# Optimization experiments

Measured on AMD Instinct MI355X. Metric: run time of the kernel, lower is better.

Reference implementation:

```python
import jax, jax.numpy as jnp
import numpy as np

# Izhikevich constants (module defaults)
A, B_P, C_P, D_P = 0.02, 0.2, -65.0, 8.0
V_TH, DT, T_STEPS = 30.0, 0.5, 8
LN_EPS = 1e-5

IN_F, OUT_F, BATCH = 4096, 4096, 256


def setup_inputs() -> dict:
    key = jax.random.key(0)
    k_x, k_w, k_n = jax.random.split(key, 3)
    x = jax.random.normal(k_x, (BATCH, IN_F), dtype=jnp.float32)
    # kaiming_normal_ fan_in / relu: std = sqrt(2 / fan_in)
    W = jax.random.normal(k_w, (OUT_F, IN_F), dtype=jnp.float32) * np.sqrt(2.0 / IN_F)
    b = jnp.zeros((OUT_F,), dtype=jnp.float32)
    ln_gamma = jnp.ones((OUT_F,), dtype=jnp.float32)
    ln_beta = jnp.zeros((OUT_F,), dtype=jnp.float32)
    current_mag = jnp.asarray(12.0, dtype=jnp.float32)
    # per-step injected noise, precomputed for determinism: (T, B, N)
    noise = jax.random.normal(k_n, (T_STEPS, BATCH, OUT_F), dtype=jnp.float32)
    return {"x": x, "W": W, "b": b, "ln_gamma": ln_gamma, "ln_beta": ln_beta,
            "current_mag": current_mag, "noise": noise}


@jax.custom_vjp
def superspike(v):
    return (v >= V_TH).astype(v.dtype)

def _ss_fwd(v):
    return superspike(v), v

def _ss_bwd(v, g):
    return (g / (1.0 + jnp.abs(v - V_TH)) ** 2,)

superspike.defvjp(_ss_fwd, _ss_bwd)


def reference(x, W, b, ln_gamma, ln_beta, current_mag, noise):
    # 1. Linear projection: (B, in) @ (in, out)
    raw = x @ W.T + b
    # 2. LayerNorm -> tanh -> scale to pA range
    mu = jnp.mean(raw, axis=-1, keepdims=True)
    var = jnp.mean(jnp.square(raw - mu), axis=-1, keepdims=True)
    ln = (raw - mu) * jax.lax.rsqrt(var + LN_EPS) * ln_gamma + ln_beta
    I_inj = jnp.tanh(ln) * jnp.abs(current_mag)  # (B, N)

    B = x.shape[0]
    v0 = jnp.full((B, OUT_F), -65.0, dtype=x.dtype)
    u0 = jnp.full((B, OUT_F), B_P * -65.0, dtype=x.dtype)

    def step(carry, noise_t):
        v, u = carry
        I_t = I_inj + 0.3 * noise_t
        dv = (0.04 * v * v + 5.0 * v + 140.0 - u + I_t) * DT
        du = A * (B_P * v - u) * DT
        v_new = jnp.clip(v + dv, -100.0, 60.0)
        u_new = jnp.clip(u + du, -100.0, 100.0)
        s = superspike(v_new)
        v_out = v_new * (1.0 - s) + C_P * s
        u_out = u_new + D_P * s
        # truncated BPTT: detach state each step
        new_carry = (jax.lax.stop_gradient(v_out), jax.lax.stop_gradient(u_out))
        return new_carry, s

    _, spikes = jax.lax.scan(step, (v0, u0), noise)  # spikes: (T, B, N)
    return jnp.sum(spikes, axis=0) / T_STEPS
```

## Files before the change

kernel.cpp:

```cpp
#include <hip/hip_runtime.h>
#include <math.h>

#define IN_F 4096
#define OUT_F 4096
#define BATCH 256
#define TSTEPS 8

#define BM 128
#define BN 64
#define BK 32
#define KSPLIT 8
#define KLEN (IN_F / KSPLIT)
#define NKT (KLEN / BK)
#define LDA 40

typedef _Float16 f16x8 __attribute__((ext_vector_type(8)));
typedef float f32x4 __attribute__((ext_vector_type(4)));

__device__ __forceinline__ void cvt8(const float4 a, const float4 b,
                                     f16x8& h0, f16x8& h1) {
  const float v[8] = {a.x, a.y, a.z, a.w, b.x, b.y, b.z, b.w};
#pragma unroll
  for (int j = 0; j < 8; ++j) {
    const float sv = v[j] * 64.0f;
    const _Float16 c0 = (_Float16)sv;
    const float r = (sv - (float)c0) * 2048.0f;
    h0[j] = c0;
    h1[j] = (_Float16)r;
  }
}

__global__ __launch_bounds__(256, 4) void gemm_split(
    const float* __restrict__ X, const float* __restrict__ Wt,
    float* __restrict__ out) {
  __shared__ __align__(16) _Float16 A0s[BM][LDA];
  __shared__ __align__(16) _Float16 A1s[BM][LDA];
  __shared__ __align__(16) _Float16 B0s[BN][LDA];
  __shared__ __align__(16) _Float16 B1s[BN][LDA];

  const int tid = threadIdx.x;
  const int lane = tid & 63;
  const int w = tid >> 6;
  const int lr = lane & 15;
  const int lk = lane >> 4;

  const int m0 = blockIdx.y * BM;
  const int n0 = blockIdx.x * BN;
  const int kbeg = blockIdx.z * KLEN;

  const int arow = tid >> 1;
  const int ako = (tid & 1) * 16;
  const int brow = tid >> 2;
  const int bko = (tid & 3) * 8;
  const float* pa = X + (size_t)(m0 + arow) * IN_F + kbeg + ako;
  const float* pb = Wt + (size_t)(n0 + brow) * IN_F + kbeg + bko;

  f32x4 acc0[2][4], acc1[2][4];
#pragma unroll
  for (int i = 0; i < 2; ++i)
#pragma unroll
    for (int j = 0; j < 4; ++j) {
      acc0[i][j] = (f32x4){0.f, 0.f, 0.f, 0.f};
      acc1[i][j] = (f32x4){0.f, 0.f, 0.f, 0.f};
    }

  for (int kt = 0; kt < NKT; ++kt) {
    const int ko = kt * BK;
    __syncthreads();
    {
      const float4 a0 = *(const float4*)(pa + ko);
      const float4 a1 = *(const float4*)(pa + ko + 4);
      const float4 a2 = *(const float4*)(pa + ko + 8);
      const float4 a3 = *(const float4*)(pa + ko + 12);
      const float4 b0 = *(const float4*)(pb + ko);
      const float4 b1 = *(const float4*)(pb + ko + 4);
      f16x8 h0, h1;
      cvt8(a0, a1, h0, h1);
      *(f16x8*)&A0s[arow][ako] = h0;
      *(f16x8*)&A1s[arow][ako] = h1;
      cvt8(a2, a3, h0, h1);
      *(f16x8*)&A0s[arow][ako + 8] = h0;
      *(f16x8*)&A1s[arow][ako + 8] = h1;
      cvt8(b0, b1, h0, h1);
      *(f16x8*)&B0s[brow][bko] = h0;
      *(f16x8*)&B1s[brow][bko] = h1;
    }
    __syncthreads();

    f16x8 fa0[2], fa1[2];
#pragma unroll
    for (int i = 0; i < 2; ++i) {
      fa0[i] = *(const f16x8*)&A0s[w * 32 + i * 16 + lr][lk * 8];
      fa1[i] = *(const f16x8*)&A1s[w * 32 + i * 16 + lr][lk * 8];
    }
#pragma unroll
    for (int j = 0; j < 4; ++j) {
      const f16x8 fb0 = *(const f16x8*)&B0s[j * 16 + lr][lk * 8];
      const f16x8 fb1 = *(const f16x8*)&B1s[j * 16 + lr][lk * 8];
#pragma unroll
      for (int i = 0; i < 2; ++i) {
        acc0[i][j] = __builtin_amdgcn_mfma_f32_16x16x32_f16(fa0[i], fb0, acc0[i][j], 0, 0, 0);
        acc1[i][j] = __builtin_amdgcn_mfma_f32_16x16x32_f16(fa0[i], fb1, acc1[i][j], 0, 0, 0);
        acc1[i][j] = __builtin_amdgcn_mfma_f32_16x16x32_f16(fa1[i], fb0, acc1[i][j], 0, 0, 0);
      }
    }
  }

#pragma unroll
  for (int i = 0; i < 2; ++i) {
    const int rbase = m0 + w * 32 + i * 16 + lk * 4;
#pragma unroll
    for (int j = 0; j < 4; ++j) {
      const int c = n0 + j * 16 + lr;
#pragma unroll
      for (int r = 0; r < 4; ++r) {
        const float val = acc0[i][j][r] * 2.44140625e-4f  +
                          acc1[i][j][r] * 1.1920928955078125e-7f ;
        atomicAdd(&out[(size_t)(rbase + r) * OUT_F + c], val);
      }
    }
  }
}

__global__ __launch_bounds__(512) void snn_fused(
    float* __restrict__ raw, const float* __restrict__ bias,
    const float* __restrict__ gamma, const float* __restrict__ beta,
    const float* __restrict__ cmag, const float* __restrict__ noise) {
  const int row = blockIdx.x;
  const int tid = threadIdx.x;
  const int lane = tid & 63;
  const int wid = tid >> 6;
  const int col = tid * 8;
  __shared__ float redS[8], redQ[8];

  float x[8];
#pragma unroll
  for (int p = 0; p < 2; ++p) {
    const float4 rv = *(const float4*)&raw[(size_t)row * OUT_F + col + p * 4];
    const float4 bv = *(const float4*)&bias[col + p * 4];
    x[p * 4 + 0] = rv.x + bv.x;
    x[p * 4 + 1] = rv.y + bv.y;
    x[p * 4 + 2] = rv.z + bv.z;
    x[p * 4 + 3] = rv.w + bv.w;
  }
  float s = 0.f, q = 0.f;
#pragma unroll
  for (int e = 0; e < 8; ++e) {
    s += x[e];
    q += x[e] * x[e];
  }
#pragma unroll
  for (int off = 32; off; off >>= 1) {
    s += __shfl_xor(s, off);
    q += __shfl_xor(q, off);
  }
  if (lane == 0) {
    redS[wid] = s;
    redQ[wid] = q;
  }
  __syncthreads();
  s = 0.f;
  q = 0.f;
#pragma unroll
  for (int wv = 0; wv < 8; ++wv) {
    s += redS[wv];
    q += redQ[wv];
  }
  const float mu = s * (1.0f / (float)OUT_F);
  const float var = q * (1.0f / (float)OUT_F) - mu * mu;
  const float sc = 1.0f / sqrtf(var + 1e-5f);
  const float mag = fabsf(cmag[0]);

  float I[8];
#pragma unroll
  for (int p = 0; p < 2; ++p) {
    const float4 g = *(const float4*)&gamma[col + p * 4];
    const float4 be = *(const float4*)&beta[col + p * 4];
    I[p * 4 + 0] = tanhf((x[p * 4 + 0] - mu) * sc * g.x + be.x) * mag;
    I[p * 4 + 1] = tanhf((x[p * 4 + 1] - mu) * sc * g.y + be.y) * mag;
    I[p * 4 + 2] = tanhf((x[p * 4 + 2] - mu) * sc * g.z + be.z) * mag;
    I[p * 4 + 3] = tanhf((x[p * 4 + 3] - mu) * sc * g.w + be.w) * mag;
  }

  float v[8], u[8];
  int cnt[8];
#pragma unroll
  for (int j = 0; j < 8; ++j) {
    v[j] = -65.0f;
    u[j] = -13.0f;
    cnt[j] = 0;
  }

#pragma unroll
  for (int t = 0; t < TSTEPS; ++t) {
    float nn[8];
#pragma unroll
    for (int p = 0; p < 2; ++p) {
      const float4 nz = *(const float4*)&noise[(((size_t)t * BATCH) + row) * OUT_F + col + p * 4];
      nn[p * 4 + 0] = nz.x;
      nn[p * 4 + 1] = nz.y;
      nn[p * 4 + 2] = nz.z;
      nn[p * 4 + 3] = nz.w;
    }
#pragma unroll
    for (int j = 0; j < 8; ++j) {
      const float It = I[j] + 0.3f * nn[j];
      const float vv = v[j];
      const float dv = (0.04f * vv * vv + 5.0f * vv + 140.0f - u[j] + It) * 0.5f;
      const float du = 0.02f * (0.2f * vv - u[j]) * 0.5f;
      float vn = vv + dv;
      vn = fminf(fmaxf(vn, -100.0f), 60.0f);
      float un = u[j] + du;
      un = fminf(fmaxf(un, -100.0f), 100.0f);
      const bool sp = (vn >= 30.0f);
      v[j] = sp ? -65.0f : vn;
      u[j] = sp ? (un + 8.0f) : un;
      cnt[j] += sp ? 1 : 0;
    }
  }

#pragma unroll
  for (int p = 0; p < 2; ++p) {
    float4 o;
    o.x = (float)cnt[p * 4 + 0] * 0.125f;
    o.y = (float)cnt[p * 4 + 1] * 0.125f;
    o.z = (float)cnt[p * 4 + 2] * 0.125f;
    o.w = (float)cnt[p * 4 + 3] * 0.125f;
    *(float4*)&raw[(size_t)row * OUT_F + col + p * 4] = o;
  }
}

extern "C" void kernel_launch(void* const* d_in, const int* in_sizes, int n_in,
                              void* d_out, int out_size, void* d_ws, size_t ws_size,
                              hipStream_t stream) {
  const float* x = (const float*)d_in[0];
  const float* W = (const float*)d_in[1];
  const float* b = (const float*)d_in[2];
  const float* gam = (const float*)d_in[3];
  const float* bet = (const float*)d_in[4];
  const float* cmag = (const float*)d_in[5];
  const float* nz = (const float*)d_in[6];
  float* out = (float*)d_out;
  (void)d_ws;
  (void)ws_size;

  hipMemsetAsync(out, 0, (size_t)BATCH * OUT_F * sizeof(float), stream);

  dim3 grid1(OUT_F / BN, BATCH / BM, KSPLIT);
  gemm_split<<<grid1, 256, 0, stream>>>(x, W, out);

  snn_fused<<<BATCH, 512, 0, stream>>>(out, b, gam, bet, cmag, nz);
}
```

Before: 184.2 us.

## Load A fragments directly from global into registers and prefetch B tile

The X (A) operand is no longer staged through shared memory. Each wave loads its own rows from global memory straight into registers and does the fp16 hi/lo split there, which removes the A LDS writes and reads. The B tile's global loads are software-prefetched one k-step ahead so they overlap the MFMA work. In exchange, global A accesses become less coalesced, since each lane reads 32 bytes from a different row, and register pressure rises, so the occupancy hint is lowered from 4 to 3 blocks per CU.

```diff
diff --git a/kernel.cpp b/kernel.cpp
--- a/kernel.cpp
+++ b/kernel.cpp
@@ -30,11 +30,9 @@
   }
 }
 
-__global__ __launch_bounds__(256, 4) void gemm_split(
+__global__ __launch_bounds__(256, 3) void gemm_split(
     const float* __restrict__ X, const float* __restrict__ Wt,
     float* __restrict__ out) {
-  __shared__ __align__(16) _Float16 A0s[BM][LDA];
-  __shared__ __align__(16) _Float16 A1s[BM][LDA];
   __shared__ __align__(16) _Float16 B0s[BN][LDA];
   __shared__ __align__(16) _Float16 B1s[BN][LDA];
 
@@ -48,11 +46,11 @@
   const int n0 = blockIdx.x * BN;
   const int kbeg = blockIdx.z * KLEN;
 
-  const int arow = tid >> 1;
-  const int ako = (tid & 1) * 16;
+  const float* paf0 = X + (size_t)(m0 + w * 32 + lr) * IN_F + kbeg + lk * 8;
+  const float* paf1 = paf0 + (size_t)16 * IN_F;
+
   const int brow = tid >> 2;
   const int bko = (tid & 3) * 8;
-  const float* pa = X + (size_t)(m0 + arow) * IN_F + kbeg + ako;
   const float* pb = Wt + (size_t)(n0 + brow) * IN_F + kbeg + bko;
 
   f32x4 acc0[2][4], acc1[2][4];
@@ -64,35 +62,33 @@
       acc1[i][j] = (f32x4){0.f, 0.f, 0.f, 0.f};
     }
 
+  float4 b0 = *(const float4*)(pb);
+  float4 b1 = *(const float4*)(pb + 4);
+
   for (int kt = 0; kt < NKT; ++kt) {
     const int ko = kt * BK;
+    const float4 a00 = *(const float4*)(paf0 + ko);
+    const float4 a01 = *(const float4*)(paf0 + ko + 4);
+    const float4 a10 = *(const float4*)(paf1 + ko);
+    const float4 a11 = *(const float4*)(paf1 + ko + 4);
+
     __syncthreads();
     {
-      const float4 a0 = *(const float4*)(pa + ko);
-      const float4 a1 = *(const float4*)(pa + ko + 4);
-      const float4 a2 = *(const float4*)(pa + ko + 8);
-      const float4 a3 = *(const float4*)(pa + ko + 12);
-      const float4 b0 = *(const float4*)(pb + ko);
-      const float4 b1 = *(const float4*)(pb + ko + 4);
       f16x8 h0, h1;
-      cvt8(a0, a1, h0, h1);
-      *(f16x8*)&A0s[arow][ako] = h0;
-      *(f16x8*)&A1s[arow][ako] = h1;
-      cvt8(a2, a3, h0, h1);
-      *(f16x8*)&A0s[arow][ako + 8] = h0;
-      *(f16x8*)&A1s[arow][ako + 8] = h1;
       cvt8(b0, b1, h0, h1);
       *(f16x8*)&B0s[brow][bko] = h0;
       *(f16x8*)&B1s[brow][bko] = h1;
     }
+    if (kt + 1 < NKT) {
+      b0 = *(const float4*)(pb + ko + BK);
+      b1 = *(const float4*)(pb + ko + BK + 4);
+    }
     __syncthreads();
 
     f16x8 fa0[2], fa1[2];
-#pragma unroll
-    for (int i = 0; i < 2; ++i) {
-      fa0[i] = *(const f16x8*)&A0s[w * 32 + i * 16 + lr][lk * 8];
-      fa1[i] = *(const f16x8*)&A1s[w * 32 + i * 16 + lr][lk * 8];
-    }
+    cvt8(a00, a01, fa0[0], fa1[0]);
+    cvt8(a10, a11, fa0[1], fa1[1]);
+
 #pragma unroll
     for (int j = 0; j < 4; ++j) {
       const f16x8 fb0 = *(const f16x8*)&B0s[j * 16 + lr][lk * 8];
```

Result: no change. 186.4 us (+1.2%).
